# Performance work log

Hardware: AMD Instinct MI355X
Metric: run time of the kernel (lower is better)

Reference implementation:

```python
import jax, jax.numpy as jnp
import numpy as np

K = 50  # top-k causal instances (UC_MIL constructor)


def setup_inputs() -> dict:
    key = jax.random.key(0)
    k1, k2 = jax.random.split(key)
    X = jax.random.normal(k1, (8, 4096, 768), dtype=jnp.float32)
    # GCN layer weight: nn.Linear(768, 1, bias=False) -> weight shape (1, 768)
    W = jax.random.normal(k2, (1, 768), dtype=jnp.float32) * 0.02
    return {"X": X, "W": W}


def reference(X, W):
    # X: (B, N, D) bag of instance features; W: (1, D) GCN weight
    B, N, D = X.shape
    k = K

    # --- build_adjacency_matrix, batched ---
    Xc = X - X.mean(axis=1, keepdims=True)                      # center over instances
    cov = jnp.einsum('bnd,bmd->bnm', Xc, Xc)                    # (B, N, N)
    var = jnp.sqrt(jnp.sum(Xc * Xc, axis=-1, keepdims=True)) + 1e-6  # (B, N, 1)
    corr = cov / (var * jnp.swapaxes(var, 1, 2))                # var @ var.T
    A = jnp.abs(corr)
    dinv = jnp.sum(A, axis=-1) ** (-0.5)                        # (B, N)
    # D @ A @ D with diagonal D == row/col scaling (same math, no dense diag)
    A_norm = dinv[:, :, None] * A * dinv[:, None, :]

    # --- 1-layer GCN score: (A_norm @ (X W^T)).squeeze(-1) ---
    XW = jnp.einsum('bnd,d->bn', X, W[0])                       # (B, N)
    S = jnp.einsum('bnm,bm->bn', A_norm, XW)                    # (B, N)

    # --- top-k causal / non-causal split, vectorized over batch ---
    _, topk_idx = jax.lax.top_k(S, k)                           # (B, k)
    F_c = jnp.take_along_axis(X, topk_idx[:, :, None], axis=1)  # (B, k, D)

    # non-topk indices in ascending order (torch.arange(N)[mask] semantics)
    flag = jnp.zeros((B, N), dtype=jnp.int32)
    flag = flag.at[jnp.arange(B)[:, None], topk_idx].set(1)
    non_idx = jnp.argsort(flag, axis=1, stable=True)[:, : N - k]  # (B, N-k)
    F_nc = jnp.take_along_axis(X, non_idx[:, :, None], axis=1)    # (B, N-k, D)

    # NOTE: original code has a bug: topk_indices = torch.stack(F_i_c, 0),
    # i.e. the second output is the gathered features, not the indices.
    # We replicate that faithfully.
    return (S,
            F_c,
            F_c.mean(axis=1, keepdims=True),
            F_nc.mean(axis=1, keepdims=True))
```

## Files before the change

### kernel.cpp

```cpp
#include <hip/hip_runtime.h>
#include <stdint.h>

typedef unsigned short u16;
typedef short bf16x8 __attribute__((ext_vector_type(8)));
typedef float f32x4 __attribute__((ext_vector_type(4)));
typedef unsigned long long ull;

#define NB 8
#define NROW 4096
#define ND 768
#define NKB 24
#define NRB 32
#define KTILE 4096
#define NTRI 528
#define TOPK 50

#define CPART_OFF 0u
#define CSUM_OFF  786432u
#define MEAN_OFF  811008u
#define RV_OFF    835584u
#define XW_OFF    966656u
#define T_OFF     1097728u
#define U_OFF     1228800u
#define SMALL_TOTAL 1359872u
#define HI_OFF    ((size_t)SMALL_TOTAL)
#define LO_OFF    (HI_OFF + 50331648ull)
#define COV_OFF   (LO_OFF + 50331648ull)

static __device__ __forceinline__ u16 f2bf(float f) {
  uint32_t u = __float_as_uint(f);
  u += 0x7FFFu + ((u >> 16) & 1u);
  return (u16)(u >> 16);
}
static __device__ __forceinline__ float bf2f(u16 h) {
  return __uint_as_float(((uint32_t)h) << 16);
}

static __device__ __forceinline__ void gload_lds16(const char* g, char* l) {
  __builtin_amdgcn_global_load_lds(
      (const __attribute__((address_space(1))) uint32_t*)(const void*)g,
      (__attribute__((address_space(3))) uint32_t*)(void*)l, 16, 0, 0);
}

static __device__ __forceinline__ int tile_swz(int t) {
  return (t & 7) * 66 + (t >> 3);
}

__global__ __launch_bounds__(256)
void colsum1_kernel(const float* __restrict__ X, float* __restrict__ part) {
  const int nc = blockIdx.x;
  const int d  = threadIdx.x + blockIdx.y * 256;
  const int b  = blockIdx.z;
  const float* p = X + ((size_t)b * NROW + (size_t)nc * 128) * ND + d;
  float s = 0.f;
  for (int i = 0; i < 128; ++i) s += p[(size_t)i * ND];
  part[((size_t)b * 32 + nc) * ND + d] = s;
}

__global__ __launch_bounds__(256)
void colsum2_kernel(const float* __restrict__ part, float* __restrict__ csum,
                    float* __restrict__ mean) {
  const int d = threadIdx.x + blockIdx.x * 256;
  const int b = blockIdx.y;
  float s = 0.f;
  for (int i = 0; i < 32; ++i) s += part[((size_t)b * 32 + i) * ND + d];
  csum[(size_t)b * ND + d] = s;
  mean[(size_t)b * ND + d] = s * (1.0f / 4096.0f);
}

__global__ __launch_bounds__(128)
void rowstats_kernel(const float* __restrict__ X, const float* __restrict__ W,
                     const float* __restrict__ mean,
                     u16* __restrict__ hi, u16* __restrict__ lo,
                     float* __restrict__ rv, float* __restrict__ xw) {
  const int n  = blockIdx.x;
  const int gb = blockIdx.y;
  const int tid = threadIdx.x;
  const float* xr = X + ((size_t)gb * NROW + n) * ND;
  const float* mb = mean + (size_t)gb * ND;
  const int r = n & 127, rbk = n >> 7;
  float ssq = 0.f, sw = 0.f;
  if (tid < 96) {
    const int d0 = tid * 8;
    const float4 xa = *(const float4*)(xr + d0);
    const float4 xb = *(const float4*)(xr + d0 + 4);
    const float4 ma = *(const float4*)(mb + d0);
    const float4 mc = *(const float4*)(mb + d0 + 4);
    const float4 wa = *(const float4*)(W + d0);
    const float4 wb = *(const float4*)(W + d0 + 4);
    float x[8]  = {xa.x, xa.y, xa.z, xa.w, xb.x, xb.y, xb.z, xb.w};
    float mm[8] = {ma.x, ma.y, ma.z, ma.w, mc.x, mc.y, mc.z, mc.w};
    float ww[8] = {wa.x, wa.y, wa.z, wa.w, wb.x, wb.y, wb.z, wb.w};
    u16 hbits[8], lbits[8];
#pragma unroll
    for (int i = 0; i < 8; ++i) {
      float xc = x[i] - mm[i];
      ssq += xc * xc;
      sw  += x[i] * ww[i];
      u16 hb = f2bf(xc);
      float hf = bf2f(hb);
      u16 lb2 = f2bf(xc - hf);
      hbits[i] = hb; lbits[i] = lb2;
    }
    const int kb = d0 >> 5;
    const int kk = d0 & 31;
    const size_t tbyte = ((size_t)((gb * NRB + rbk) * NKB + kb)) * 8192
                       + (size_t)((r * 64 + kk * 2) ^ ((r & 7) << 4));
    uint4 hv, lv;
    hv.x = (uint32_t)hbits[0] | ((uint32_t)hbits[1] << 16);
    hv.y = (uint32_t)hbits[2] | ((uint32_t)hbits[3] << 16);
    hv.z = (uint32_t)hbits[4] | ((uint32_t)hbits[5] << 16);
    hv.w = (uint32_t)hbits[6] | ((uint32_t)hbits[7] << 16);
    lv.x = (uint32_t)lbits[0] | ((uint32_t)lbits[1] << 16);
    lv.y = (uint32_t)lbits[2] | ((uint32_t)lbits[3] << 16);
    lv.z = (uint32_t)lbits[4] | ((uint32_t)lbits[5] << 16);
    lv.w = (uint32_t)lbits[6] | ((uint32_t)lbits[7] << 16);
    *(uint4*)((char*)hi + tbyte) = hv;
    *(uint4*)((char*)lo + tbyte) = lv;
  }
#pragma unroll
  for (int m = 1; m < 64; m <<= 1) {
    ssq += __shfl_xor(ssq, m, 64);
    sw  += __shfl_xor(sw, m, 64);
  }
  __shared__ float sh[4];
  const int w = tid >> 6, lane = tid & 63;
  if (lane == 0) { sh[w * 2] = ssq; sh[w * 2 + 1] = sw; }
  __syncthreads();
  if (tid == 0) {
    float S = sh[0] + sh[2];
    float T = sh[1] + sh[3];
    const size_t i = (size_t)gb * NROW + n;
    rv[i] = 1.0f / (sqrtf(S) + 1e-6f);
    xw[i] = T;
  }
}

static __device__ __forceinline__ bf16x8 read_frag(const u16* sm, int r, int kbyte) {
  const int byte = (r * 64 + kbyte) ^ ((r & 7) << 4);
  return *(const bf16x8*)((const char*)sm + byte);
}

__attribute__((always_inline))
static __device__ void dev_gemm(int bx, int gb,
                                const u16* __restrict__ hi, const u16* __restrict__ lo,
                                const float* __restrict__ coef,
                                float* __restrict__ outacc, float* __restrict__ covout) {
  const int tsw = tile_swz(bx);
  int trem = tsw;
  int rb = 0;
  while (trem >= NRB - rb) { trem -= NRB - rb; ++rb; }
  const int cb = rb + trem;

  __shared__ u16 sm[4 * KTILE];
  u16* aHi = sm;
  u16* bHi = sm + KTILE;
  u16* aLo = sm + 2 * KTILE;
  u16* bLo = sm + 3 * KTILE;

  const int tid = threadIdx.x;
  const int lane = tid & 63;
  const int wid = tid >> 6;
  const int wrow = wid >> 1, wcol = wid & 1;
  const int l15 = lane & 15, lg = lane >> 4;

  const char* hA = (const char*)(hi + (size_t)((gb * NRB + rb) * NKB) * KTILE);
  const char* hB = (const char*)(hi + (size_t)((gb * NRB + cb) * NKB) * KTILE);
  const char* lA = (const char*)(lo + (size_t)((gb * NRB + rb) * NKB) * KTILE);
  const char* lB = (const char*)(lo + (size_t)((gb * NRB + cb) * NKB) * KTILE);

  f32x4 acc[4][4];
#pragma unroll
  for (int i = 0; i < 4; ++i)
#pragma unroll
    for (int j = 0; j < 4; ++j) acc[i][j] = f32x4{0.f, 0.f, 0.f, 0.f};

  for (int kb = 0; kb < NKB; ++kb) {
    __syncthreads();
    const size_t kb8 = (size_t)kb * 8192;
#pragma unroll
    for (int it = 0; it < 2; ++it) {
      const int off = it * 4096 + tid * 16;
      gload_lds16(hA + kb8 + off, (char*)aHi + off);
      gload_lds16(hB + kb8 + off, (char*)bHi + off);
      gload_lds16(lA + kb8 + off, (char*)aLo + off);
      gload_lds16(lB + kb8 + off, (char*)bLo + off);
    }
    __syncthreads();

    bf16x8 ah[4], bh[4], al[4], bl[4];
#pragma unroll
    for (int i = 0; i < 4; ++i) {
      ah[i] = read_frag(aHi, wrow * 64 + i * 16 + l15, lg * 16);
      bh[i] = read_frag(bHi, wcol * 64 + i * 16 + l15, lg * 16);
      al[i] = read_frag(aLo, wrow * 64 + i * 16 + l15, lg * 16);
      bl[i] = read_frag(bLo, wcol * 64 + i * 16 + l15, lg * 16);
    }
#pragma unroll
    for (int mi = 0; mi < 4; ++mi)
#pragma unroll
      for (int ni = 0; ni < 4; ++ni) {
        acc[mi][ni] = __builtin_amdgcn_mfma_f32_16x16x32_bf16(ah[mi], bh[ni], acc[mi][ni], 0, 0, 0);
        acc[mi][ni] = __builtin_amdgcn_mfma_f32_16x16x32_bf16(ah[mi], bl[ni], acc[mi][ni], 0, 0, 0);
        acc[mi][ni] = __builtin_amdgcn_mfma_f32_16x16x32_bf16(al[mi], bh[ni], acc[mi][ni], 0, 0, 0);
      }
  }

  const float* cf = coef + (size_t)gb * NROW;
  float* oa = outacc + (size_t)gb * NROW;
  const int rbase = rb * 128 + wrow * 64;
  const int cbase = cb * 128 + wcol * 64;

  float* cv = covout + ((size_t)gb * NTRI + tsw) * 16384;
#pragma unroll
  for (int mi = 0; mi < 4; ++mi)
#pragma unroll
    for (int ni = 0; ni < 4; ++ni)
#pragma unroll
      for (int j = 0; j < 4; ++j)
        cv[(wrow * 64 + mi * 16 + lg * 4 + j) * 128 + wcol * 64 + ni * 16 + l15] =
            fabsf(acc[mi][ni][j]);

  float ccol[4];
#pragma unroll
  for (int ni = 0; ni < 4; ++ni) ccol[ni] = cf[cbase + ni * 16 + l15];

  float rs[4][4];
#pragma unroll
  for (int mi = 0; mi < 4; ++mi)
#pragma unroll
    for (int j = 0; j < 4; ++j) {
      float s = 0.f;
#pragma unroll
      for (int ni = 0; ni < 4; ++ni) s += fabsf(acc[mi][ni][j]) * ccol[ni];
      rs[mi][j] = s;
    }
#pragma unroll
  for (int m = 1; m < 16; m <<= 1)
#pragma unroll
    for (int mi = 0; mi < 4; ++mi)
#pragma unroll
      for (int j = 0; j < 4; ++j) rs[mi][j] += __shfl_xor(rs[mi][j], m, 64);
  if (l15 == 0) {
#pragma unroll
    for (int mi = 0; mi < 4; ++mi)
#pragma unroll
      for (int j = 0; j < 4; ++j)
        atomicAdd(&oa[rbase + mi * 16 + lg * 4 + j], rs[mi][j]);
  }

  if (rb != cb) {
    float crow[4][4];
#pragma unroll
    for (int mi = 0; mi < 4; ++mi)
#pragma unroll
      for (int j = 0; j < 4; ++j) crow[mi][j] = cf[rbase + mi * 16 + lg * 4 + j];
    float cs[4];
#pragma unroll
    for (int ni = 0; ni < 4; ++ni) {
      float s = 0.f;
#pragma unroll
      for (int mi = 0; mi < 4; ++mi)
#pragma unroll
        for (int j = 0; j < 4; ++j) s += fabsf(acc[mi][ni][j]) * crow[mi][j];
      cs[ni] = s;
    }
#pragma unroll
    for (int ni = 0; ni < 4; ++ni) {
      cs[ni] += __shfl_xor(cs[ni], 16, 64);
      cs[ni] += __shfl_xor(cs[ni], 32, 64);
    }
    if (lg == 0) {
#pragma unroll
      for (int ni = 0; ni < 4; ++ni)
        atomicAdd(&oa[cbase + ni * 16 + l15], cs[ni]);
    }
  }
}

__attribute__((always_inline))
static __device__ void dev_upass(int bx, int gb,
                                 const float* __restrict__ cov, const float* __restrict__ tt,
                                 const float* __restrict__ rv, const float* __restrict__ xw,
                                 float* __restrict__ uacc) {
  const int tsw = tile_swz(bx);
  int trem = tsw;
  int rb = 0;
  while (trem >= NRB - rb) { trem -= NRB - rb; ++rb; }
  const int cb = rb + trem;

  const float* A = cov + ((size_t)gb * NTRI + tsw) * 16384;
  const size_t bo = (size_t)gb * NROW;

  __shared__ float wr[128];
  __shared__ float rsum[128];
  __shared__ float csum_p[8][128];

  const int t = threadIdx.x;
  const int g = t >> 5;
  const int l = t & 31;

  if (t < 128) {
    const int row = rb * 128 + t;
    wr[t] = (1.0f / sqrtf(rv[bo + row] * tt[bo + row])) * xw[bo + row] * rv[bo + row];
  }
  float4 wc4;
  {
    const int col = cb * 128 + l * 4;
    const float4 r4 = *(const float4*)(rv + bo + col);
    const float4 t4 = *(const float4*)(tt + bo + col);
    const float4 x4 = *(const float4*)(xw + bo + col);
    wc4.x = (1.0f / sqrtf(r4.x * t4.x)) * x4.x * r4.x;
    wc4.y = (1.0f / sqrtf(r4.y * t4.y)) * x4.y * r4.y;
    wc4.z = (1.0f / sqrtf(r4.z * t4.z)) * x4.z * r4.z;
    wc4.w = (1.0f / sqrtf(r4.w * t4.w)) * x4.w * r4.w;
  }
  __syncthreads();

  float sc0 = 0.f, sc1 = 0.f, sc2 = 0.f, sc3 = 0.f;
#pragma unroll
  for (int i = 0; i < 16; ++i) {
    const int r = g + i * 8;
    const float4 v = *(const float4*)(A + r * 128 + l * 4);
    float p = v.x * wc4.x + v.y * wc4.y + v.z * wc4.z + v.w * wc4.w;
    const float wrr = wr[r];
    sc0 += v.x * wrr; sc1 += v.y * wrr; sc2 += v.z * wrr; sc3 += v.w * wrr;
#pragma unroll
    for (int m = 1; m < 32; m <<= 1) p += __shfl_xor(p, m, 64);
    if (l == 0) rsum[r] = p;
  }
  csum_p[g][l * 4 + 0] = sc0;
  csum_p[g][l * 4 + 1] = sc1;
  csum_p[g][l * 4 + 2] = sc2;
  csum_p[g][l * 4 + 3] = sc3;
  __syncthreads();

  float* ua = uacc + bo;
  if (t < 128) atomicAdd(&ua[rb * 128 + t], rsum[t]);
  if (rb != cb && t < 128) {
    float s = 0.f;
#pragma unroll
    for (int gg = 0; gg < 8; ++gg) s += csum_p[gg][t];
    atomicAdd(&ua[cb * 128 + t], s);
  }
}

__global__ __launch_bounds__(256, 2)
void gemm_kernel(const u16* __restrict__ hi, const u16* __restrict__ lo,
                 const float* __restrict__ rv, float* __restrict__ tacc,
                 float* __restrict__ cov, int b0) {
  dev_gemm(blockIdx.x, b0 + blockIdx.y, hi, lo, rv, tacc, cov);
}

__global__ __launch_bounds__(256, 2)
void upass_kernel(const float* __restrict__ cov, const float* __restrict__ tacc,
                  const float* __restrict__ rv, const float* __restrict__ xw,
                  float* __restrict__ uacc, int b0) {
  dev_upass(blockIdx.x, b0 + blockIdx.y, cov, tacc, rv, xw, uacc);
}

__global__ __launch_bounds__(256, 2)
void fused_kernel(const u16* __restrict__ hi, const u16* __restrict__ lo,
                  const float* __restrict__ rv, const float* __restrict__ xw,
                  float* __restrict__ tacc, float* __restrict__ uacc,
                  float* __restrict__ cov, int ng, int bg0, int bu0) {
  if ((int)blockIdx.y < ng)
    dev_gemm(blockIdx.x, bg0 + blockIdx.y, hi, lo, rv, tacc, cov);
  else
    dev_upass(blockIdx.x, bu0 + blockIdx.y - ng, cov, tacc, rv, xw, uacc);
}

__global__ __launch_bounds__(1024)
void topk_kernel(const float* __restrict__ tt, const float* __restrict__ rv,
                 const float* __restrict__ u, const float* __restrict__ X,
                 const float* __restrict__ csum, float* __restrict__ S,
                 float* __restrict__ outFc, float* __restrict__ outC,
                 float* __restrict__ outNC) {
  const int b = blockIdx.x;
  __shared__ ull keys[NROW];
  __shared__ ull wred[16];
  __shared__ int selLds[TOPK];
  const int t = threadIdx.x;
  const int lane = t & 63, w = t >> 6;
  const size_t bo = (size_t)b * NROW;
#pragma unroll
  for (int j = 0; j < 4; ++j) {
    const int i = t + j * 1024;
    const float rvi = rv[bo + i];
    const float s = (1.0f / sqrtf(rvi * tt[bo + i])) * rvi * u[bo + i];
    S[bo + i] = s;
    uint32_t uu = __float_as_uint(s);
    uu = (uu & 0x80000000u) ? ~uu : (uu | 0x80000000u);
    keys[i] = ((ull)uu << 32) | (uint32_t)(4095 - i);
  }
  __syncthreads();
  for (int r = 0; r < TOPK; ++r) {
    ull m = keys[t];
    ull m2 = keys[t + 1024]; if (m2 > m) m = m2;
    m2 = keys[t + 2048]; if (m2 > m) m = m2;
    m2 = keys[t + 3072]; if (m2 > m) m = m2;
#pragma unroll
    for (int sh = 1; sh < 64; sh <<= 1) {
      ull o = __shfl_xor(m, sh, 64);
      if (o > m) m = o;
    }
    if (lane == 0) wred[w] = m;
    __syncthreads();
    if (w == 0) {
      ull mm = wred[lane & 15];
#pragma unroll
      for (int sh = 1; sh < 16; sh <<= 1) {
        ull o = __shfl_xor(mm, sh, 64);
        if (o > mm) mm = o;
      }
      if (lane == 0) {
        const int sel = 4095 - (int)(mm & 0xFFFFFFFFu);
        selLds[r] = sel;
        keys[sel] = 0ULL;
      }
    }
    __syncthreads();
  }

  if (t < ND) {
    float s = 0.f;
    for (int r = 0; r < TOPK; ++r) {
      const int row = selLds[r];
      const float v = X[(bo + row) * ND + t];
      outFc[((size_t)b * TOPK + r) * ND + t] = v;
      s += v;
    }
    outC[(size_t)b * ND + t]  = s * (1.0f / 50.0f);
    outNC[(size_t)b * ND + t] = (csum[(size_t)b * ND + t] - s) * (1.0f / 4046.0f);
  }
}

extern "C" void kernel_launch(void* const* d_in, const int* in_sizes, int n_in,
                              void* d_out, int out_size, void* d_ws, size_t ws_size,
                              hipStream_t stream) {
  const float* X = (const float*)d_in[0];
  const float* W = (const float*)d_in[1];
  float* out = (float*)d_out;
  char* ws = (char*)d_ws;

  float* cpart = (float*)(ws + CPART_OFF);
  float* csum  = (float*)(ws + CSUM_OFF);
  float* mean  = (float*)(ws + MEAN_OFF);
  float* rv    = (float*)(ws + RV_OFF);
  float* xw    = (float*)(ws + XW_OFF);
  float* tacc  = (float*)(ws + T_OFF);
  float* uacc  = (float*)(ws + U_OFF);
  u16* hi      = (u16*)(ws + HI_OFF);
  u16* lo      = (u16*)(ws + LO_OFF);
  float* cov   = (float*)(ws + COV_OFF);

  float* outS  = out;
  float* outFc = out + 32768;
  float* outMC = out + 339968;
  float* outMN = out + 346112;

  hipMemsetAsync(ws + T_OFF, 0, 262144, stream);

  colsum1_kernel<<<dim3(32, 3, NB), 256, 0, stream>>>(X, cpart);
  colsum2_kernel<<<dim3(3, NB), 256, 0, stream>>>(cpart, csum, mean);
  rowstats_kernel<<<dim3(NROW, NB), 128, 0, stream>>>(X, W, mean, hi, lo, rv, xw);

  gemm_kernel<<<dim3(NTRI, 6), 256, 0, stream>>>(hi, lo, rv, tacc, cov, 0);
  fused_kernel<<<dim3(NTRI, 8), 256, 0, stream>>>(hi, lo, rv, xw, tacc, uacc, cov,
                                                  2, 6, 0);
  upass_kernel<<<dim3(NTRI, 2), 256, 0, stream>>>(cov, tacc, rv, xw, uacc, 6);

  topk_kernel<<<NB, 1024, 0, stream>>>(tacc, rv, uacc, X, csum, outS, outFc, outMC, outMN);
}
```

Before: 506.3 us.

## Replace staggered gemm/upass overlap with two full-batch kernels and nontemporal cov traffic

```diff
diff --git a/kernel.cpp b/kernel.cpp
--- a/kernel.cpp
+++ b/kernel.cpp
@@ -141,12 +141,12 @@
   return *(const bf16x8*)((const char*)sm + byte);
 }
 
-__attribute__((always_inline))
-static __device__ void dev_gemm(int bx, int gb,
-                                const u16* __restrict__ hi, const u16* __restrict__ lo,
-                                const float* __restrict__ coef,
-                                float* __restrict__ outacc, float* __restrict__ covout) {
-  const int tsw = tile_swz(bx);
+__global__ __launch_bounds__(256, 2)
+void gemm_acc_kernel(const u16* __restrict__ hi, const u16* __restrict__ lo,
+                     const float* __restrict__ coef, float* __restrict__ outacc,
+                     float* __restrict__ covout) {
+  const int gb = blockIdx.y;
+  const int tsw = tile_swz(blockIdx.x);
   int trem = tsw;
   int rb = 0;
   while (trem >= NRB - rb) { trem -= NRB - rb; ++rb; }
@@ -218,8 +218,9 @@
     for (int ni = 0; ni < 4; ++ni)
 #pragma unroll
       for (int j = 0; j < 4; ++j)
-        cv[(wrow * 64 + mi * 16 + lg * 4 + j) * 128 + wcol * 64 + ni * 16 + l15] =
-            fabsf(acc[mi][ni][j]);
+        __builtin_nontemporal_store(
+            fabsf(acc[mi][ni][j]),
+            cv + (wrow * 64 + mi * 16 + lg * 4 + j) * 128 + wcol * 64 + ni * 16 + l15);
 
   float ccol[4];
 #pragma unroll
@@ -278,12 +279,12 @@
   }
 }
 
-__attribute__((always_inline))
-static __device__ void dev_upass(int bx, int gb,
-                                 const float* __restrict__ cov, const float* __restrict__ tt,
-                                 const float* __restrict__ rv, const float* __restrict__ xw,
-                                 float* __restrict__ uacc) {
-  const int tsw = tile_swz(bx);
+__global__ __launch_bounds__(256, 2)
+void upass_kernel(const float* __restrict__ cov, const float* __restrict__ tt,
+                  const float* __restrict__ rv, const float* __restrict__ xw,
+                  float* __restrict__ uacc) {
+  const int gb = blockIdx.y;
+  const int tsw = tile_swz(blockIdx.x);
   int trem = tsw;
   int rb = 0;
   while (trem >= NRB - rb) { trem -= NRB - rb; ++rb; }
@@ -293,7 +294,7 @@
   const size_t bo = (size_t)gb * NROW;
 
   __shared__ float wr[128];
-  __shared__ float rsum[128];
+  __shared__ float plds[128 * 33];
   __shared__ float csum_p[8][128];
 
   const int t = threadIdx.x;
@@ -321,13 +322,10 @@
 #pragma unroll
   for (int i = 0; i < 16; ++i) {
     const int r = g + i * 8;
-    const float4 v = *(const float4*)(A + r * 128 + l * 4);
-    float p = v.x * wc4.x + v.y * wc4.y + v.z * wc4.z + v.w * wc4.w;
+    const f32x4 v = __builtin_nontemporal_load((const f32x4*)(A + r * 128 + l * 4));
+    plds[r * 33 + l] = v[0] * wc4.x + v[1] * wc4.y + v[2] * wc4.z + v[3] * wc4.w;
     const float wrr = wr[r];
-    sc0 += v.x * wrr; sc1 += v.y * wrr; sc2 += v.z * wrr; sc3 += v.w * wrr;
-#pragma unroll
-    for (int m = 1; m < 32; m <<= 1) p += __shfl_xor(p, m, 64);
-    if (l == 0) rsum[r] = p;
+    sc0 += v[0] * wrr; sc1 += v[1] * wrr; sc2 += v[2] * wrr; sc3 += v[3] * wrr;
   }
   csum_p[g][l * 4 + 0] = sc0;
   csum_p[g][l * 4 + 1] = sc1;
@@ -336,38 +334,18 @@
   __syncthreads();
 
   float* ua = uacc + bo;
-  if (t < 128) atomicAdd(&ua[rb * 128 + t], rsum[t]);
-  if (rb != cb && t < 128) {
-    float s = 0.f;
-#pragma unroll
-    for (int gg = 0; gg < 8; ++gg) s += csum_p[gg][t];
-    atomicAdd(&ua[cb * 128 + t], s);
-  }
-}
-
-__global__ __launch_bounds__(256, 2)
-void gemm_kernel(const u16* __restrict__ hi, const u16* __restrict__ lo,
-                 const float* __restrict__ rv, float* __restrict__ tacc,
-                 float* __restrict__ cov, int b0) {
-  dev_gemm(blockIdx.x, b0 + blockIdx.y, hi, lo, rv, tacc, cov);
-}
-
-__global__ __launch_bounds__(256, 2)
-void upass_kernel(const float* __restrict__ cov, const float* __restrict__ tacc,
-                  const float* __restrict__ rv, const float* __restrict__ xw,
-                  float* __restrict__ uacc, int b0) {
-  dev_upass(blockIdx.x, b0 + blockIdx.y, cov, tacc, rv, xw, uacc);
-}
-
-__global__ __launch_bounds__(256, 2)
-void fused_kernel(const u16* __restrict__ hi, const u16* __restrict__ lo,
-                  const float* __restrict__ rv, const float* __restrict__ xw,
-                  float* __restrict__ tacc, float* __restrict__ uacc,
-                  float* __restrict__ cov, int ng, int bg0, int bu0) {
-  if ((int)blockIdx.y < ng)
-    dev_gemm(blockIdx.x, bg0 + blockIdx.y, hi, lo, rv, tacc, cov);
-  else
-    dev_upass(blockIdx.x, bu0 + blockIdx.y - ng, cov, tacc, rv, xw, uacc);
+  if (t < 128) {
+    float rsum = 0.f;
+#pragma unroll
+    for (int i = 0; i < 32; ++i) rsum += plds[t * 33 + i];
+    atomicAdd(&ua[rb * 128 + t], rsum);
+    if (rb != cb) {
+      float s = 0.f;
+#pragma unroll
+      for (int gg = 0; gg < 8; ++gg) s += csum_p[gg][t];
+      atomicAdd(&ua[cb * 128 + t], s);
+    }
+  }
 }
 
 __global__ __launch_bounds__(1024)
@@ -464,11 +442,7 @@
   colsum1_kernel<<<dim3(32, 3, NB), 256, 0, stream>>>(X, cpart);
   colsum2_kernel<<<dim3(3, NB), 256, 0, stream>>>(cpart, csum, mean);
   rowstats_kernel<<<dim3(NROW, NB), 128, 0, stream>>>(X, W, mean, hi, lo, rv, xw);
-
-  gemm_kernel<<<dim3(NTRI, 6), 256, 0, stream>>>(hi, lo, rv, tacc, cov, 0);
-  fused_kernel<<<dim3(NTRI, 8), 256, 0, stream>>>(hi, lo, rv, xw, tacc, uacc, cov,
-                                                  2, 6, 0);
-  upass_kernel<<<dim3(NTRI, 2), 256, 0, stream>>>(cov, tacc, rv, xw, uacc, 6);
-
+  gemm_acc_kernel<<<dim3(NTRI, NB), 256, 0, stream>>>(hi, lo, rv, tacc, cov);
+  upass_kernel<<<dim3(NTRI, NB), 256, 0, stream>>>(cov, tacc, rv, xw, uacc);
   topk_kernel<<<NB, 1024, 0, stream>>>(tacc, rv, uacc, X, csum, outS, outFc, outMC, outMN);
 }
```

Result: faster. 460.5 us (-9.1%).
